# Kernel tuning notes

Measured on AMD Instinct MI355X. Metric: run time of the kernel, lower is better.

## Reference

```python
import jax, jax.numpy as jnp
import numpy as np

NUM_GROUPS = 32
EPS = 1e-5
HT_MIN = -1.0
HT_MAX = 1.0


def setup_inputs() -> dict:
    key = jax.random.key(0)
    k1, k2, k3 = jax.random.split(key, 3)
    B, IN, OUT = 8192, 2048, 4096
    x = jax.random.normal(k1, (B, IN), dtype=jnp.float32)
    # kaiming-uniform-ish scale for weight, uniform bias in [-1/sqrt(fan_in), 1/sqrt(fan_in)]
    bound_w = np.sqrt(1.0 / IN)
    weight = jax.random.uniform(k2, (OUT, IN), dtype=jnp.float32, minval=-bound_w, maxval=bound_w)
    bias = jax.random.uniform(k3, (OUT,), dtype=jnp.float32, minval=-bound_w, maxval=bound_w)
    return {"x": x, "weight": weight, "bias": bias}


def reference(x, weight, bias):
    # GEMM + bias: (B, out)
    y = jnp.einsum('bi,oi->bo', x, weight) + bias
    B, OUT = y.shape
    fpg = OUT // NUM_GROUPS
    g = y.reshape(B, NUM_GROUPS, fpg)
    mean = jnp.mean(g, axis=-1, keepdims=True)
    var = jnp.mean(jnp.square(g - mean), axis=-1, keepdims=True)  # biased variance
    x_hat = (g - mean) / jnp.sqrt(var + EPS)
    out = jnp.clip(x_hat, HT_MIN, HT_MAX)
    return out.reshape(B, OUT)
```

## Files before the change

### kernel.cpp

```cpp
#include <hip/hip_runtime.h>
#include <hip/hip_bf16.h>

#define B_ROWS   8192
#define K_DIM    2048
#define OUT_COLS 4096
#define EPS      1e-5f

#define BM 256
#define BN 256
#define BK 64
#define NT (K_DIM / BK)

using f32x4  = __attribute__((ext_vector_type(4))) float;
using bf16x8 = __attribute__((ext_vector_type(8))) short;

__device__ __forceinline__ unsigned short f2bf_rn(float f) {
    unsigned u = __builtin_bit_cast(unsigned, f);
    u += 0x7FFFu + ((u >> 16) & 1u);
    return (unsigned short)(u >> 16);
}

__global__ void cvt_all(const float* __restrict__ x, const float* __restrict__ w,
                        unsigned short* __restrict__ xb, unsigned short* __restrict__ wb) {
    const int n4x = (B_ROWS * K_DIM) / 4;
    const int n4w = (OUT_COLS * K_DIM) / 4;
    int stride = gridDim.x * blockDim.x;
    for (int i = blockIdx.x * blockDim.x + threadIdx.x; i < n4x + n4w; i += stride) {
        const float4* src; ushort4* dst; int j;
        if (i < n4x) { src = (const float4*)x; dst = (ushort4*)xb; j = i; }
        else         { src = (const float4*)w; dst = (ushort4*)wb; j = i - n4x; }
        float4 v = src[j];
        ushort4 r;
        r.x = f2bf_rn(v.x); r.y = f2bf_rn(v.y); r.z = f2bf_rn(v.z); r.w = f2bf_rn(v.w);
        dst[j] = r;
    }
}

__device__ __forceinline__ void gload16(const unsigned short* src, unsigned short* lds) {
    __builtin_amdgcn_global_load_lds((const __attribute__((address_space(1))) void*)src,
                                     (__attribute__((address_space(3))) void*)lds,
                                     16, 0, 0);
}

__device__ __forceinline__ float rowsum16(float v) {
    int x;
    x = __builtin_amdgcn_update_dpp(0, __builtin_bit_cast(int, v), 0x121, 0xF, 0xF, true);
    v += __builtin_bit_cast(float, x);
    x = __builtin_amdgcn_update_dpp(0, __builtin_bit_cast(int, v), 0x122, 0xF, 0xF, true);
    v += __builtin_bit_cast(float, x);
    x = __builtin_amdgcn_update_dpp(0, __builtin_bit_cast(int, v), 0x124, 0xF, 0xF, true);
    v += __builtin_bit_cast(float, x);
    x = __builtin_amdgcn_update_dpp(0, __builtin_bit_cast(int, v), 0x128, 0xF, 0xF, true);
    v += __builtin_bit_cast(float, x);
    return v;
}

#define STA(BUF, H, KT) do {                                                        \
    gload16(Ag + (H)*262144 + (KT)*64 + goff0, &As[BUF][(H)*8192 + lds0]);          \
    gload16(Ag + (H)*262144 + (KT)*64 + goff1, &As[BUF][(H)*8192 + lds1]);          \
  } while (0)
#define STB(BUF, H, KT) do {                                                        \
    gload16(Bg + (H)*262144 + (KT)*64 + goff0, &Bs[BUF][(H)*8192 + lds0]);          \
    gload16(Bg + (H)*262144 + (KT)*64 + goff1, &Bs[BUF][(H)*8192 + lds1]);          \
  } while (0)

#define RD_BH(DST, CURB, KK) do {                                                   \
    _Pragma("unroll") for (int n = 0; n < 4; ++n) {                                 \
      const int ro = browb + n * 16 * BK;                                           \
      DST[n][KK] = *(const bf16x8*)&(CURB)[ro + ((KK) ? colsw1 : colsw0)];          \
    } } while (0)

#define RD_A(CURA, Q) do {                                                          \
    _Pragma("unroll") for (int dm = 0; dm < 2; ++dm) {                              \
      const int ro = arow + (2*(Q)+dm) * 16 * BK;                                   \
      af[dm][0] = *(const bf16x8*)&(CURA)[ro + colsw0];                             \
      af[dm][1] = *(const bf16x8*)&(CURA)[ro + colsw1];                             \
    } } while (0)

#define MFMAQ(BB, Q) do {                                                           \
    _Pragma("unroll") for (int kk = 0; kk < 2; ++kk)                                \
      _Pragma("unroll") for (int dm = 0; dm < 2; ++dm)                              \
        _Pragma("unroll") for (int n = 0; n < 4; ++n)                               \
          acc[2*(Q)+dm][n] = __builtin_amdgcn_mfma_f32_16x16x32_bf16(               \
              af[dm][kk], BB[n][kk], acc[2*(Q)+dm][n], 0, 0, 0);                    \
  } while (0)

#define VW4  asm volatile("s_waitcnt vmcnt(4)" ::: "memory")
#define BAR  __builtin_amdgcn_s_barrier()

#define PH(PRERD, STAGE, MFMAS, TAILW) do {                                         \
    PRERD; STAGE;                                                                   \
    __builtin_amdgcn_s_barrier();                                                   \
    asm volatile("s_waitcnt lgkmcnt(0)" ::: "memory");                              \
    __builtin_amdgcn_sched_barrier(0);                                              \
    __builtin_amdgcn_s_setprio(1);                                                  \
    MFMAS;                                                                          \
    __builtin_amdgcn_s_setprio(0);                                                  \
    TAILW;                                                                          \
    __builtin_amdgcn_s_barrier();                                                   \
  } while (0)

#define NOP_ ((void)0)

__global__ __launch_bounds__(512, 2) void gemm_gn(const unsigned short* __restrict__ A,
                                                  const unsigned short* __restrict__ Bw,
                                                  const float* __restrict__ bias,
                                                  float* __restrict__ out) {
    __shared__ __align__(16) unsigned short As[2][16384];
    __shared__ __align__(16) unsigned short Bs[2][16384];
    __shared__ __align__(16) float redbuf[256 * 8];

    const int tid  = threadIdx.x;
    const int lane = tid & 63;
    const int wave = tid >> 6;
    const int wr   = wave >> 2;
    const int wcn  = wave & 3;
    const int l16  = lane & 15;
    const int lhi  = lane >> 4;

    const int bid  = blockIdx.x;
    const int swz  = (bid & 7) * (gridDim.x >> 3) + (bid >> 3);
    const int brow = swz >> 4;
    const int bcol = swz & 15;

    int goff0, goff1, lds0, lds1;
    {
        int f0 = tid;          int r0 = f0 >> 3;
        int f1 = 512 + tid;    int r1 = f1 >> 3;
        goff0 = r0 * K_DIM + (((f0 & 7) ^ (r0 & 7)) * 8);
        goff1 = r1 * K_DIM + (((f1 & 7) ^ (r1 & 7)) * 8);
        lds0  = f0 * 8;
        lds1  = f1 * 8;
    }
    const unsigned short* Ag = A  + (size_t)brow * BM * K_DIM;
    const unsigned short* Bg = Bw + (size_t)bcol * BN * K_DIM;

    const int colsw0 = (0 * 32 + lhi * 8) ^ ((l16 & 7) << 3);
    const int colsw1 = (1 * 32 + lhi * 8) ^ ((l16 & 7) << 3);
    const int arow   = (wr * 128 + l16) * BK;
    const int browb  = (wcn * 64 + l16) * BK;

    const unsigned short* A0p = &As[0][0];
    const unsigned short* A1p = &As[1][0];
    const unsigned short* B0p = &Bs[0][0];
    const unsigned short* B1p = &Bs[1][0];

    f32x4 acc[8][4];
    {
        float bv[4];
        #pragma unroll
        for (int n = 0; n < 4; ++n)
            bv[n] = bias[bcol * BN + wcn * 64 + n * 16 + l16];
        #pragma unroll
        for (int m = 0; m < 8; ++m)
            #pragma unroll
            for (int n = 0; n < 4; ++n)
                #pragma unroll
                for (int j = 0; j < 4; ++j)
                    acc[m][n][j] = bv[n];
    }

    bf16x8 af[2][2];
    bf16x8 bbA[4][2];
    bf16x8 bbB[4][2];

    STA(0, 0, 0); STA(0, 1, 0);
    STB(0, 0, 0); STB(0, 1, 0);
    STB(1, 0, 1); STB(1, 1, 1);
    VW4;
    BAR;
    RD_BH(bbA, B0p, 0); RD_BH(bbA, B0p, 1);

    #pragma unroll 1
    for (int tt = 0; tt < NT; tt += 2) {
        const int k1 = (tt + 1) & (NT - 1);
        const int k2 = (tt + 2) & (NT - 1);
        const int k3 = (tt + 3) & (NT - 1);
        PH( RD_A(A0p, 0),                     STA(1,0,k1); STA(1,1,k1),  MFMAQ(bbA, 0), NOP_ );
        PH( RD_A(A0p, 1),                     STB(0,0,k2); STB(0,1,k2),  MFMAQ(bbA, 1), VW4  );
        PH( RD_A(A0p, 2); RD_BH(bbB, B1p, 0), NOP_,                      MFMAQ(bbA, 2), NOP_ );
        PH( RD_A(A0p, 3); RD_BH(bbB, B1p, 1), NOP_,                      MFMAQ(bbA, 3), NOP_ );
        PH( RD_A(A1p, 0),                     STA(0,0,k2); STA(0,1,k2),  MFMAQ(bbB, 0), NOP_ );
        PH( RD_A(A1p, 1),                     STB(1,0,k3); STB(1,1,k3),  MFMAQ(bbB, 1), VW4  );
        PH( RD_A(A1p, 2); RD_BH(bbA, B0p, 0), NOP_,                      MFMAQ(bbB, 2), NOP_ );
        PH( RD_A(A1p, 3); RD_BH(bbA, B0p, 1), NOP_,                      MFMAQ(bbB, 3), NOP_ );
    }

    #pragma unroll
    for (int m = 0; m < 8; ++m) {
        #pragma unroll
        for (int j = 0; j < 4; ++j) {
            float s = 0.f, s2 = 0.f;
            #pragma unroll
            for (int n = 0; n < 4; ++n) {
                float v = acc[m][n][j];
                s += v; s2 += v * v;
            }
            s  = rowsum16(s);
            s2 = rowsum16(s2);
            if (l16 == 0) {
                int r = wr * 128 + m * 16 + lhi * 4 + j;
                redbuf[r * 8 + wcn * 2 + 0] = s;
                redbuf[r * 8 + wcn * 2 + 1] = s2;
            }
        }
    }
    asm volatile("s_waitcnt vmcnt(0)" ::: "memory");
    __syncthreads();

    const int p2 = (wcn & 2) * 2;
    #pragma unroll
    for (int m = 0; m < 8; ++m) {
        #pragma unroll
        for (int j = 0; j < 4; ++j) {
            const int r = wr * 128 + m * 16 + lhi * 4 + j;
            const float4 q = *(const float4*)&redbuf[r * 8 + p2];
            const float mean = (q.x + q.z) * (1.0f / 128.0f);
            const float var  = (q.y + q.w) * (1.0f / 128.0f) - mean * mean;
            const float rstd = rsqrtf(var + EPS);
            float* orow = out + (size_t)(brow * BM + r) * OUT_COLS + bcol * BN + wcn * 64 + l16;
            #pragma unroll
            for (int n = 0; n < 4; ++n) {
                float v = (acc[m][n][j] - mean) * rstd;
                v = fminf(fmaxf(v, -1.0f), 1.0f);
                orow[n * 16] = v;
            }
        }
    }
}

extern "C" void kernel_launch(void* const* d_in, const int* in_sizes, int n_in,
                              void* d_out, int out_size, void* d_ws, size_t ws_size,
                              hipStream_t stream) {
    const float* x    = (const float*)d_in[0];
    const float* w    = (const float*)d_in[1];
    const float* bias = (const float*)d_in[2];
    float* out        = (float*)d_out;

    unsigned short* xb = (unsigned short*)d_ws;
    unsigned short* wb = xb + (size_t)B_ROWS * K_DIM;

    cvt_all<<<3072, 256, 0, stream>>>(x, w, xb, wb);

    dim3 grid((B_ROWS / BM) * (OUT_COLS / BN));
    gemm_gn<<<grid, 512, 0, stream>>>(xb, wb, bias, out);
}
```

Measured before the change: 170.5 us.

## Spread global stage loads across all phases and drop explicit LDS wait

Rebalances the GEMM main loop so each of the eight phases issues one half-tile global-to-LDS load instead of clustering loads in four phases. Adds a vmcnt wait every second phase. Removes the explicit lgkmcnt(0) wait before the MFMA block and makes the A fragment registers phase-local, leaving the compiler to insert LDS waits. This is meant to even out memory traffic and overlap LDS reads with MFMAs, but the more frequent waits and compiler-inserted waits could stall or serialise the schedule.

Measured after the change: 176.1 us. 1.03x slower.

```diff
diff --git a/kernel.cpp b/kernel.cpp
--- a/kernel.cpp
+++ b/kernel.cpp
@@ -70,37 +70,31 @@
       DST[n][KK] = *(const bf16x8*)&(CURB)[ro + ((KK) ? colsw1 : colsw0)];          \
     } } while (0)
 
-#define RD_A(CURA, Q) do {                                                          \
+#define VW4  asm volatile("s_waitcnt vmcnt(4)" ::: "memory")
+#define BAR  __builtin_amdgcn_s_barrier()
+#define NOP_ ((void)0)
+
+#define PH(CURA, Q, BB, XRD, STAGE, TAILW) do {                                     \
+    bf16x8 af[2][2];                                                                \
     _Pragma("unroll") for (int dm = 0; dm < 2; ++dm) {                              \
       const int ro = arow + (2*(Q)+dm) * 16 * BK;                                   \
       af[dm][0] = *(const bf16x8*)&(CURA)[ro + colsw0];                             \
       af[dm][1] = *(const bf16x8*)&(CURA)[ro + colsw1];                             \
-    } } while (0)
-
-#define MFMAQ(BB, Q) do {                                                           \
+    }                                                                               \
+    XRD;                                                                            \
+    STAGE;                                                                          \
+    __builtin_amdgcn_s_barrier();                                                   \
+    __builtin_amdgcn_sched_barrier(0);                                              \
+    __builtin_amdgcn_s_setprio(1);                                                  \
     _Pragma("unroll") for (int kk = 0; kk < 2; ++kk)                                \
       _Pragma("unroll") for (int dm = 0; dm < 2; ++dm)                              \
         _Pragma("unroll") for (int n = 0; n < 4; ++n)                               \
           acc[2*(Q)+dm][n] = __builtin_amdgcn_mfma_f32_16x16x32_bf16(               \
               af[dm][kk], BB[n][kk], acc[2*(Q)+dm][n], 0, 0, 0);                    \
-  } while (0)
-
-#define VW4  asm volatile("s_waitcnt vmcnt(4)" ::: "memory")
-#define BAR  __builtin_amdgcn_s_barrier()
-
-#define PH(PRERD, STAGE, MFMAS, TAILW) do {                                         \
-    PRERD; STAGE;                                                                   \
-    __builtin_amdgcn_s_barrier();                                                   \
-    asm volatile("s_waitcnt lgkmcnt(0)" ::: "memory");                              \
-    __builtin_amdgcn_sched_barrier(0);                                              \
-    __builtin_amdgcn_s_setprio(1);                                                  \
-    MFMAS;                                                                          \
     __builtin_amdgcn_s_setprio(0);                                                  \
     TAILW;                                                                          \
     __builtin_amdgcn_s_barrier();                                                   \
   } while (0)
-
-#define NOP_ ((void)0)
 
 __global__ __launch_bounds__(512, 2) void gemm_gn(const unsigned short* __restrict__ A,
                                                   const unsigned short* __restrict__ Bw,
@@ -160,7 +154,6 @@
                     acc[m][n][j] = bv[n];
     }
 
-    bf16x8 af[2][2];
     bf16x8 bbA[4][2];
     bf16x8 bbB[4][2];
 
@@ -176,14 +169,14 @@
         const int k1 = (tt + 1) & (NT - 1);
         const int k2 = (tt + 2) & (NT - 1);
         const int k3 = (tt + 3) & (NT - 1);
-        PH( RD_A(A0p, 0),                     STA(1,0,k1); STA(1,1,k1),  MFMAQ(bbA, 0), NOP_ );
-        PH( RD_A(A0p, 1),                     STB(0,0,k2); STB(0,1,k2),  MFMAQ(bbA, 1), VW4  );
-        PH( RD_A(A0p, 2); RD_BH(bbB, B1p, 0), NOP_,                      MFMAQ(bbA, 2), NOP_ );
-        PH( RD_A(A0p, 3); RD_BH(bbB, B1p, 1), NOP_,                      MFMAQ(bbA, 3), NOP_ );
-        PH( RD_A(A1p, 0),                     STA(0,0,k2); STA(0,1,k2),  MFMAQ(bbB, 0), NOP_ );
-        PH( RD_A(A1p, 1),                     STB(1,0,k3); STB(1,1,k3),  MFMAQ(bbB, 1), VW4  );
-        PH( RD_A(A1p, 2); RD_BH(bbA, B0p, 0), NOP_,                      MFMAQ(bbB, 2), NOP_ );
-        PH( RD_A(A1p, 3); RD_BH(bbA, B0p, 1), NOP_,                      MFMAQ(bbB, 3), NOP_ );
+        PH(A0p, 0, bbA, NOP_,              STA(1, 0, k1), NOP_);
+        PH(A0p, 1, bbA, NOP_,              STA(1, 1, k1), VW4 );
+        PH(A0p, 2, bbA, RD_BH(bbB, B1p, 0), STB(0, 0, k2), NOP_);
+        PH(A0p, 3, bbA, RD_BH(bbB, B1p, 1), STB(0, 1, k2), VW4 );
+        PH(A1p, 0, bbB, NOP_,              STA(0, 0, k2), NOP_);
+        PH(A1p, 1, bbB, NOP_,              STA(0, 1, k2), VW4 );
+        PH(A1p, 2, bbB, RD_BH(bbA, B0p, 0), STB(1, 0, k3), NOP_);
+        PH(A1p, 3, bbB, RD_BH(bbA, B0p, 1), STB(1, 1, k3), VW4 );
     }
 
     #pragma unroll
```
